# Kernel tuning notes

Hardware: AMD Instinct MI355X
Metric: run time of the kernel (lower is better)

Reference implementation:

```python
import jax, jax.numpy as jnp
import numpy as np

H, HKV, D, HID = 64, 8, 64, 2880
T = 2048
WINDOW = 128
THETA = 150000.0
FACTOR = 32.0
ORIG_MAX = 4096
BETA_FAST, BETA_SLOW = 32.0, 1.0
EPS = 1e-5
SCALE = D ** -0.5
MSCALE = float(0.1 * np.log(FACTOR) + 1.0)  # vLLM YaRN attention mscale


def _yarn_inv_freq():
    # vLLM YaRNScalingRotaryEmbedding inverse frequencies
    def corr_dim(n_rot):
        return D * np.log(ORIG_MAX / (n_rot * 2.0 * np.pi)) / (2.0 * np.log(THETA))
    low = max(int(np.floor(corr_dim(BETA_FAST))), 0)
    high = min(int(np.ceil(corr_dim(BETA_SLOW))), D - 1)
    pow_ = np.arange(0, D, 2, dtype=np.float32) / D
    extrap = 1.0 / (THETA ** pow_)                 # extrapolation inv_freq
    interp = extrap / FACTOR                        # interpolation inv_freq
    ramp = np.clip((np.arange(D // 2, dtype=np.float32) - low) / max(high - low, 1e-3), 0.0, 1.0)
    extrap_mask = 1.0 - ramp
    inv_freq = interp * (1.0 - extrap_mask) + extrap * extrap_mask
    return jnp.asarray(inv_freq, jnp.float32)

_INV_FREQ = _yarn_inv_freq()


def _rope(positions, x):
    # neox-style rotation; x: [T, heads, D]
    freqs = positions.astype(jnp.float32)[:, None] * _INV_FREQ[None, :]  # [T, D/2]
    cos = (jnp.cos(freqs) * MSCALE)[:, None, :]
    sin = (jnp.sin(freqs) * MSCALE)[:, None, :]
    x1, x2 = x[..., : D // 2], x[..., D // 2 :]
    return jnp.concatenate([x1 * cos - x2 * sin, x2 * cos + x1 * sin], axis=-1)


def _attn(q, k, v, sinks):
    # q: [T,H,D]; k,v: [T,HKV,D]; sinks: [H] extra softmax logit per head
    g = H // HKV
    k = jnp.repeat(k, g, axis=1)
    v = jnp.repeat(v, g, axis=1)
    scores = jnp.einsum('qhd,khd->hqk', q, k) * SCALE  # [H,T,T]
    i = jnp.arange(T)[:, None]
    j = jnp.arange(T)[None, :]
    mask = (j <= i) & (i - j < WINDOW)  # causal + sliding window (even layer)
    scores = jnp.where(mask[None], scores, -jnp.inf)
    s = sinks[:, None]                                    # [H,1]
    m = jnp.maximum(jnp.max(scores, axis=-1), s)          # [H,T]
    p = jnp.exp(scores - m[..., None])                    # [H,T,T]
    denom = jnp.sum(p, axis=-1) + jnp.exp(s - m)          # sink adds to denominator only
    out = jnp.einsum('hqk,khd->qhd', p, v) / denom.T[..., None]
    return out.reshape(T, H * D)


def setup_inputs() -> dict:
    key = jax.random.key(0)
    ks = jax.random.split(key, 8)
    return {
        'hidden_states': jax.random.normal(ks[0], (T, HID), jnp.float32),
        'positions': jnp.arange(T, dtype=jnp.int32),
        'norm_w': jnp.ones((HID,), jnp.float32),
        'w_qkv': jax.random.normal(ks[1], ((H + 2 * HKV) * D, HID), jnp.float32) * 0.02,
        'b_qkv': jax.random.normal(ks[2], ((H + 2 * HKV) * D,), jnp.float32) * 0.02,
        'w_o': jax.random.normal(ks[3], (HID, H * D), jnp.float32) * 0.02,
        'b_o': jax.random.normal(ks[4], (HID,), jnp.float32) * 0.02,
        'sinks': jax.random.normal(ks[5], (H,), jnp.float32),
    }


def reference(hidden_states, positions, norm_w, w_qkv, b_qkv, w_o, b_o, sinks):
    x = hidden_states
    t = x * jax.lax.rsqrt(jnp.mean(x * x, axis=-1, keepdims=True) + EPS) * norm_w  # RMSNorm
    qkv = t @ w_qkv.T + b_qkv
    q, k, v = jnp.split(qkv, [H * D, H * D + HKV * D], axis=-1)
    q = _rope(positions, q.reshape(T, H, D))
    k = _rope(positions, k.reshape(T, HKV, D))
    v = v.reshape(T, HKV, D)
    attn_out = _attn(q, k, v, sinks)
    out = attn_out @ w_o.T + b_o
    return out + x  # residual
```

## Files before the change

### kernel.cpp

```cpp
#include <hip/hip_runtime.h>
#include <hip/hip_bf16.h>
#include <stdint.h>

typedef __attribute__((ext_vector_type(8))) short bf16x8;
typedef __attribute__((ext_vector_type(8))) unsigned short u16x8;
typedef __attribute__((ext_vector_type(4))) float f32x4;
typedef __attribute__((ext_vector_type(4))) unsigned short u16x4;

#define T_SEQ 2048
#define HID_D 2880
#define KPAD 2944
#define NH 64
#define NKV 8
#define HD 64
#define QKV_N 5120
#define ATT_N 4096
#define NOPAD 3072
#define WIN 128
#define RSCALE 0.125f
#define MSCALE 1.3465735903f
#define ROPE_TOT (T_SEQ * (NH + NKV) * 32)

__device__ __forceinline__ unsigned short f2bf(float f) {
  union { float f; unsigned u; } v; v.f = f;
  unsigned r = v.u + 0x7fffu + ((v.u >> 16) & 1u);
  return (unsigned short)(r >> 16);
}
__device__ __forceinline__ float bf2f(unsigned short u) {
  union { unsigned u; float f; } v; v.u = ((unsigned)u) << 16;
  return v.f;
}

__device__ __forceinline__ void gload_lds16(const void* g, void* l) {
  __builtin_amdgcn_global_load_lds((const __attribute__((address_space(1))) char*)g,
                                   (__attribute__((address_space(3))) char*)l, 16, 0, 0);
}

#define GPH_MID()                                        \
  __builtin_amdgcn_s_barrier();                          \
  asm volatile("s_waitcnt lgkmcnt(0)" ::: "memory");     \
  __builtin_amdgcn_sched_barrier(0);                     \
  __builtin_amdgcn_s_setprio(1)
#define GPH_END()                                        \
  __builtin_amdgcn_s_setprio(0);                         \
  __builtin_amdgcn_s_barrier()

__global__ __launch_bounds__(256) void pre_kernel(const float* __restrict__ x,
                                                  const float* __restrict__ w,
                                                  unsigned short* __restrict__ t_bf,
                                                  const float* __restrict__ wq_src,
                                                  unsigned short* __restrict__ wq_dst) {
  __shared__ float red[256];
  if (blockIdx.x < 2048) {
    int row = blockIdx.x;
    const float4* xr4 = (const float4*)(x + (size_t)row * HID_D);
    const float4* w4 = (const float4*)w;
    float ss = 0.f;
    for (int i = threadIdx.x; i < 720; i += 256) {
      float4 v = xr4[i];
      ss += v.x * v.x + v.y * v.y + v.z * v.z + v.w * v.w;
    }
    red[threadIdx.x] = ss;
    __syncthreads();
    for (int s = 128; s > 0; s >>= 1) {
      if (threadIdx.x < s) red[threadIdx.x] += red[threadIdx.x + s];
      __syncthreads();
    }
    float rs = rsqrtf(red[0] / (float)HID_D + 1e-5f);
    u16x4* ob = (u16x4*)(t_bf + (size_t)row * KPAD);
    for (int i = threadIdx.x; i < 736; i += 256) {
      u16x4 o = {0, 0, 0, 0};
      if (i < 720) {
        float4 v = xr4[i];
        float4 g = w4[i];
        o = { f2bf(v.x * rs * g.x), f2bf(v.y * rs * g.y),
              f2bf(v.z * rs * g.z), f2bf(v.w * rs * g.w) };
      }
      ob[i] = o;
    }
  } else {
    const int total = QKV_N * 736;
    for (int i = (blockIdx.x - 2048) * 256 + threadIdx.x; i < total; i += 1024 * 256) {
      int c4 = i % 736, row = i / 736;
      u16x4 o = {0, 0, 0, 0};
      if (c4 < 720) {
        float4 v = ((const float4*)wq_src)[(size_t)row * 720 + c4];
        o = { f2bf(v.x), f2bf(v.y), f2bf(v.z), f2bf(v.w) };
      }
      ((u16x4*)wq_dst)[i] = o;
    }
  }
}

__global__ __launch_bounds__(512, 2) void qkv320_kernel(const unsigned short* __restrict__ A,
                                                        const unsigned short* __restrict__ B,
                                                        unsigned short* __restrict__ C,
                                                        const float* __restrict__ bias) {
  __shared__ unsigned short sA[2 * 128 * 64];
  __shared__ unsigned short sB[3 * 320 * 64];

  const int tid = threadIdx.x;
  const int lane = tid & 63, wid = tid >> 6;
  const int wr = wid >> 2, wc = wid & 3;
  const int lq = lane & 15, ro = lane >> 4;

  const int c = blockIdx.x & 7, q = blockIdx.x >> 3;
  const int by = (c & 1) * 8 + (q & 7);
  const int bx = (c >> 1) * 4 + (q >> 3);
  const int m0 = by * 128, n0 = bx * 320;

  const int R0 = tid >> 3;
  const int g0 = (((tid & 7) ^ (R0 & 7)) << 3);
  const size_t aOff = (size_t)(m0 + R0) * KPAD + g0;
  size_t bOff[5];
#pragma unroll
  for (int r = 0; r < 5; ++r)
    bOff[r] = (size_t)(n0 + r * 64 + R0) * KPAD + g0;

  const int ck0 = ((ro ^ (lq & 7)) << 3);
  const int ck1 = (((4 + ro) ^ (lq & 7)) << 3);

#define QSTG_A(BUF, KT)                                                         \
  { unsigned short* _d = sA + (BUF) * 8192 + wid * 512;                         \
    const unsigned short* _s = A + aOff + (size_t)(KT) * 64;                    \
    gload_lds16(_s, _d); gload_lds16(_s + (size_t)64 * KPAD, _d + 4096); }
#define QSTG_B(BUF, KT)                                                         \
  { unsigned short* _d = sB + (BUF) * 20480 + wid * 512;                        \
    gload_lds16(B + bOff[0] + (KT) * 64, _d);                                   \
    gload_lds16(B + bOff[1] + (KT) * 64, _d + 4096);                            \
    gload_lds16(B + bOff[2] + (KT) * 64, _d + 8192);                            \
    gload_lds16(B + bOff[3] + (KT) * 64, _d + 12288);                           \
    gload_lds16(B + bOff[4] + (KT) * 64, _d + 16384); }

  bf16x8 aR[8];
  bf16x8 b00, b01, b10, b11, b20, b21, b30, b31, b40, b41;
  f32x4 acc[4][5] = {};

#define QLDA(BUF)                                                                          \
  { _Pragma("unroll") for (int ii = 0; ii < 4; ++ii) {                                     \
      const int _r = (BUF) * 8192 + (wr * 64 + ii * 16 + lq) * 64;                         \
      aR[ii * 2 + 0] = *(const bf16x8*)&sA[_r + ck0];                                      \
      aR[ii * 2 + 1] = *(const bf16x8*)&sA[_r + ck1]; } }
#define QLDB(BUF, J, D0, D1)                                                               \
  { const int _r = (BUF) * 20480 + (wc * 80 + (J) * 16 + lq) * 64;                         \
    D0 = *(const bf16x8*)&sB[_r + ck0];                                                    \
    D1 = *(const bf16x8*)&sB[_r + ck1]; }
#define QMM(J, B0, B1)                                                                     \
  { _Pragma("unroll") for (int ii = 0; ii < 4; ++ii) {                                     \
      acc[ii][J] = __builtin_amdgcn_mfma_f32_16x16x32_bf16(aR[ii * 2 + 0], B0, acc[ii][J], 0, 0, 0); \
      acc[ii][J] = __builtin_amdgcn_mfma_f32_16x16x32_bf16(aR[ii * 2 + 1], B1, acc[ii][J], 0, 0, 0); } }

  QSTG_B(0, 0); QSTG_A(0, 0);
  QSTG_B(1, 1); QSTG_A(1, 1);
  asm volatile("s_waitcnt vmcnt(7)" ::: "memory");
  __builtin_amdgcn_s_barrier();

  const int nt = 46;
  for (int T = 0; T < nt; ++T) {
    const bool more = (T + 2 < nt);
    const int bb = T % 3, bA = T & 1;
    QLDA(bA);
    QLDB(bb, 0, b00, b01);
    QLDB(bb, 1, b10, b11);
    if (more) QSTG_B((T + 2) % 3, T + 2);
    GPH_MID();
    QMM(0, b00, b01);
    QMM(1, b10, b11);
    GPH_END();
    QLDB(bb, 2, b20, b21);
    QLDB(bb, 3, b30, b31);
    QLDB(bb, 4, b40, b41);
    if (more) QSTG_A((T + 2) & 1, T + 2);
    GPH_MID();
    QMM(2, b20, b21);
    QMM(3, b30, b31);
    QMM(4, b40, b41);
    __builtin_amdgcn_s_setprio(0);
    if (more) asm volatile("s_waitcnt vmcnt(7)" ::: "memory");
    else      asm volatile("s_waitcnt vmcnt(0)" ::: "memory");
    __builtin_amdgcn_s_barrier();
  }
#undef QSTG_A
#undef QSTG_B
#undef QLDA
#undef QLDB
#undef QMM

#pragma unroll
  for (int ii = 0; ii < 4; ++ii) {
    const int gr = m0 + wr * 64 + ii * 16 + ro * 4;
#pragma unroll
    for (int j = 0; j < 5; ++j) {
      const int gc = n0 + wc * 80 + j * 16 + lq;
      const float bv = bias[gc];
#pragma unroll
      for (int r = 0; r < 4; ++r)
        C[(size_t)(gr + r) * QKV_N + gc] = f2bf(acc[ii][j][r] + bv);
    }
  }
}

__global__ __launch_bounds__(512, 2) void outproj192_kernel(const unsigned short* __restrict__ att,
                                                            const unsigned short* __restrict__ wo,
                                                            float* __restrict__ out,
                                                            const float* __restrict__ b_o,
                                                            const float* __restrict__ x) {
  __shared__ unsigned short sA[3 * 128 * 64];
  __shared__ unsigned short sB[3 * 192 * 64];

  const int tid = threadIdx.x;
  const int lane = tid & 63, wid = tid >> 6;
  const int wr = wid >> 2, wc = wid & 3;
  const int lq = lane & 15, ro = lane >> 4;

  const int c = blockIdx.x & 7, q = blockIdx.x >> 3;
  const int by = c * 2 + (q >= 15 ? 1 : 0);
  const int bx = (q >= 15) ? q - 15 : q;
  const int m0 = by * 128, n0 = bx * 192;

  const int R0 = tid >> 3;
  const int g0 = (((tid & 7) ^ (R0 & 7)) << 3);
  const size_t aOff = (size_t)(m0 + R0) * ATT_N + g0;
  size_t bOff[3];
#pragma unroll
  for (int r = 0; r < 3; ++r)
    bOff[r] = (size_t)(n0 + r * 64 + R0) * ATT_N + g0;

  const int ck0 = ((ro ^ (lq & 7)) << 3);
  const int ck1 = (((4 + ro) ^ (lq & 7)) << 3);

#define PSTG_A(BUF, KT)                                                         \
  { unsigned short* _d = sA + (BUF) * 8192 + wid * 512;                         \
    const unsigned short* _s = att + aOff + (size_t)(KT) * 64;                  \
    gload_lds16(_s, _d); gload_lds16(_s + (size_t)64 * ATT_N, _d + 4096); }
#define PSTG_B(BUF, KT)                                                         \
  { unsigned short* _d = sB + (BUF) * 12288 + wid * 512;                        \
    gload_lds16(wo + bOff[0] + (KT) * 64, _d);                                  \
    gload_lds16(wo + bOff[1] + (KT) * 64, _d + 4096);                           \
    gload_lds16(wo + bOff[2] + (KT) * 64, _d + 8192); }

  bf16x8 aR[8];
  bf16x8 b00, b01, b10, b11, b20, b21;
  f32x4 acc[4][3] = {};

#define PLDA(BUF)                                                                          \
  { _Pragma("unroll") for (int ii = 0; ii < 4; ++ii) {                                     \
      const int _r = (BUF) * 8192 + (wr * 64 + ii * 16 + lq) * 64;                         \
      aR[ii * 2 + 0] = *(const bf16x8*)&sA[_r + ck0];                                      \
      aR[ii * 2 + 1] = *(const bf16x8*)&sA[_r + ck1]; } }
#define PLDB(BUF, J, D0, D1)                                                               \
  { const int _r = (BUF) * 12288 + (wc * 48 + (J) * 16 + lq) * 64;                         \
    D0 = *(const bf16x8*)&sB[_r + ck0];                                                    \
    D1 = *(const bf16x8*)&sB[_r + ck1]; }

  PSTG_B(0, 0); PSTG_A(0, 0);
  PSTG_B(1, 1); PSTG_A(1, 1);
  asm volatile("s_waitcnt vmcnt(5)" ::: "memory");
  __builtin_amdgcn_s_barrier();

  const int nt = 64;
  for (int T = 0; T < nt; ++T) {
    const bool more = (T + 2 < nt);
    const int bb = T % 3;
    PLDA(bb);
    PLDB(bb, 0, b00, b01);
    PLDB(bb, 1, b10, b11);
    PLDB(bb, 2, b20, b21);
    if (more) { PSTG_B((T + 2) % 3, T + 2); PSTG_A((T + 2) % 3, T + 2); }
    GPH_MID();
#pragma unroll
    for (int ii = 0; ii < 4; ++ii) {
      acc[ii][0] = __builtin_amdgcn_mfma_f32_16x16x32_bf16(aR[ii * 2 + 0], b00, acc[ii][0], 0, 0, 0);
      acc[ii][0] = __builtin_amdgcn_mfma_f32_16x16x32_bf16(aR[ii * 2 + 1], b01, acc[ii][0], 0, 0, 0);
      acc[ii][1] = __builtin_amdgcn_mfma_f32_16x16x32_bf16(aR[ii * 2 + 0], b10, acc[ii][1], 0, 0, 0);
      acc[ii][1] = __builtin_amdgcn_mfma_f32_16x16x32_bf16(aR[ii * 2 + 1], b11, acc[ii][1], 0, 0, 0);
      acc[ii][2] = __builtin_amdgcn_mfma_f32_16x16x32_bf16(aR[ii * 2 + 0], b20, acc[ii][2], 0, 0, 0);
      acc[ii][2] = __builtin_amdgcn_mfma_f32_16x16x32_bf16(aR[ii * 2 + 1], b21, acc[ii][2], 0, 0, 0);
    }
    __builtin_amdgcn_s_setprio(0);
    if (more) asm volatile("s_waitcnt vmcnt(5)" ::: "memory");
    else      asm volatile("s_waitcnt vmcnt(0)" ::: "memory");
    __builtin_amdgcn_s_barrier();
  }
#undef PSTG_A
#undef PSTG_B
#undef PLDA
#undef PLDB

#pragma unroll
  for (int ii = 0; ii < 4; ++ii) {
    const int gr = m0 + wr * 64 + ii * 16 + ro * 4;
#pragma unroll
    for (int j = 0; j < 3; ++j) {
      const int gc = n0 + wc * 48 + j * 16 + lq;
      const float bv = b_o[gc];
#pragma unroll
      for (int r = 0; r < 4; ++r) {
        size_t off = (size_t)(gr + r) * HID_D + gc;
        out[off] = acc[ii][j][r] + bv + x[off];
      }
    }
  }
}

__global__ __launch_bounds__(256) void ropev_kernel(const unsigned short* __restrict__ qkvb,
                                                    const int* __restrict__ positions,
                                                    unsigned short* __restrict__ qb,
                                                    unsigned short* __restrict__ kb) {
  int idx = blockIdx.x * 256 + threadIdx.x;
  int d = idx & 31;
  int head = (idx >> 5) % (NH + NKV);
  int t = idx / ((NH + NKV) * 32);
  float pw = (float)d * (1.0f / 32.0f);
  float extrap = expf(-pw * 11.9183905733f);
  float interp = extrap * (1.0f / 32.0f);
  float ramp = fminf(fmaxf(((float)d - 8.0f) * 0.1f, 0.0f), 1.0f);
  float invf = interp * ramp + extrap * (1.0f - ramp);
  float fr = (float)positions[t] * invf;
  float s, c;
  sincosf(fr, &s, &c);
  c *= MSCALE;
  s *= MSCALE;
  if (head < NH) {
    const unsigned short* b = qkvb + (size_t)t * QKV_N + head * HD + d;
    float x1 = bf2f(b[0]), x2 = bf2f(b[32]);
    unsigned short* ob = qb + (size_t)t * ATT_N + head * HD + d;
    ob[0] = f2bf(x1 * c - x2 * s);
    ob[32] = f2bf(x2 * c + x1 * s);
  } else {
    int gk = head - NH;
    const unsigned short* b = qkvb + (size_t)t * QKV_N + NH * HD + gk * HD + d;
    float x1 = bf2f(b[0]), x2 = bf2f(b[32]);
    unsigned short* ob = kb + (size_t)t * (NKV * HD) + gk * HD + d;
    ob[0] = f2bf(x1 * c - x2 * s);
    ob[32] = f2bf(x2 * c + x1 * s);
  }
}

__global__ __launch_bounds__(256) void vtrans_kernel(const unsigned short* __restrict__ qkvb,
                                                     unsigned short* __restrict__ vt) {
  __shared__ unsigned short tile[64][72];
  const int g = blockIdx.x >> 5;
  const int t0 = (blockIdx.x & 31) << 6;
  const int r = threadIdx.x >> 3;
  const int c8 = (threadIdx.x & 7) << 3;
  const size_t vbase = (size_t)(NH + NKV) * HD + (size_t)g * HD;
#pragma unroll
  for (int hh = 0; hh < 2; ++hh) {
    int row = r + hh * 32;
    *(u16x8*)&tile[row][c8] =
        *(const u16x8*)(qkvb + (size_t)(t0 + row) * QKV_N + vbase + c8);
  }
  __syncthreads();
  const int d = threadIdx.x >> 2;
  const int ts = (threadIdx.x & 3) << 4;
  u16x8 v0, v1;
#pragma unroll
  for (int i = 0; i < 8; ++i) { v0[i] = tile[ts + i][d]; v1[i] = tile[ts + 8 + i][d]; }
  unsigned short* dst = vt + (size_t)(g * HD + d) * T_SEQ + t0 + ts;
  *(u16x8*)dst = v0;
  *(u16x8*)(dst + 8) = v1;
}

__global__ __launch_bounds__(256) void attn_kernel(const unsigned short* __restrict__ qb,
                                                   const unsigned short* __restrict__ kb,
                                                   const unsigned short* __restrict__ vt,
                                                   const float* __restrict__ sinks,
                                                   unsigned short* __restrict__ att,
                                                   const float* __restrict__ wo_src,
                                                   unsigned short* __restrict__ wo_dst) {
  __shared__ unsigned short orep[4][16][72];
  {
    const int bid = blockIdx.y * gridDim.x + blockIdx.x;
    const int total = HID_D * 1024;
    for (int i = bid * 256 + threadIdx.x; i < total; i += 2048 * 256) {
      float4 v = ((const float4*)wo_src)[i];
      u16x4 o = { f2bf(v.x), f2bf(v.y), f2bf(v.z), f2bf(v.w) };
      ((u16x4*)wo_dst)[i] = o;
    }
  }
  const int lane = threadIdx.x & 63;
  const int wid = threadIdx.x >> 6;
  const int q0 = blockIdx.x * 16;
  const int h = blockIdx.y * 4 + wid;
  const int g = h >> 3;
  const int lq = lane & 15;
  const int ro = lane >> 4;

  bf16x8 bq0, bq1;
  {
    const unsigned short* qp = qb + (size_t)(q0 + lq) * ATT_N + h * HD + ro * 8;
    bq0 = *(const bf16x8*)qp;
    bq1 = *(const bf16x8*)(qp + 32);
  }
  float m_run = sinks[h];
  float l_run = 1.0f;
  f32x4 o0 = {0.f, 0.f, 0.f, 0.f}, o1 = o0, o2 = o0, o3 = o0;
  const int qg = q0 + lq;
  const int jstart = (q0 >= WIN) ? q0 - WIN : 0;

  for (int jt = jstart; jt <= q0; jt += 32) {
    f32x4 st0 = {0.f, 0.f, 0.f, 0.f}, st1 = st0;
    {
      int kr = jt + ((lq >> 2) << 3) + (lq & 3);
      int kr0 = min(kr, T_SEQ - 1);
      int kr1 = min(kr + 4, T_SEQ - 1);
      const unsigned short* kp0 = kb + (size_t)kr0 * (NKV * HD) + g * HD + ro * 8;
      const unsigned short* kp1 = kb + (size_t)kr1 * (NKV * HD) + g * HD + ro * 8;
      bf16x8 ka0a = *(const bf16x8*)kp0;
      bf16x8 ka0b = *(const bf16x8*)(kp0 + 32);
      bf16x8 ka1a = *(const bf16x8*)kp1;
      bf16x8 ka1b = *(const bf16x8*)(kp1 + 32);
      st0 = __builtin_amdgcn_mfma_f32_16x16x32_bf16(ka0a, bq0, st0, 0, 0, 0);
      st0 = __builtin_amdgcn_mfma_f32_16x16x32_bf16(ka0b, bq1, st0, 0, 0, 0);
      st1 = __builtin_amdgcn_mfma_f32_16x16x32_bf16(ka1a, bq0, st1, 0, 0, 0);
      st1 = __builtin_amdgcn_mfma_f32_16x16x32_bf16(ka1b, bq1, st1, 0, 0, 0);
    }
    float p[8];
    float tmax = -3.0e30f;
#pragma unroll
    for (int r = 0; r < 4; ++r) {
      int jg0 = jt + ro * 8 + r;
      int jg1 = jg0 + 4;
      float s0 = (jg0 <= qg && (qg - jg0) < WIN) ? st0[r] * RSCALE : -3.0e30f;
      float s1 = (jg1 <= qg && (qg - jg1) < WIN) ? st1[r] * RSCALE : -3.0e30f;
      p[r] = s0;
      p[r + 4] = s1;
      tmax = fmaxf(tmax, fmaxf(s0, s1));
    }
    tmax = fmaxf(tmax, __shfl_xor(tmax, 16));
    tmax = fmaxf(tmax, __shfl_xor(tmax, 32));
    float m_new = fmaxf(m_run, tmax);
    float rescale = expf(m_run - m_new);
    float psum = 0.f;
    bf16x8 pa;
#pragma unroll
    for (int jj = 0; jj < 8; ++jj) {
      float pe = expf(p[jj] - m_new);
      psum += pe;
      pa[jj] = (short)f2bf(pe);
    }
    psum += __shfl_xor(psum, 16);
    psum += __shfl_xor(psum, 32);
    l_run = l_run * rescale + psum;
    m_run = m_new;
    f32x4 rs4;
#pragma unroll
    for (int r = 0; r < 4; ++r) rs4[r] = __shfl(rescale, ro * 4 + r);
    o0 *= rs4; o1 *= rs4; o2 *= rs4; o3 *= rs4;
    int tb = jt + ro * 8;
    if (tb > T_SEQ - 8) tb = T_SEQ - 8;
    const unsigned short* vp = vt + (size_t)(g * HD + lq) * T_SEQ + tb;
    bf16x8 v0 = *(const bf16x8*)vp;
    bf16x8 v1 = *(const bf16x8*)(vp + 16 * T_SEQ);
    bf16x8 v2 = *(const bf16x8*)(vp + 32 * T_SEQ);
    bf16x8 v3 = *(const bf16x8*)(vp + 48 * T_SEQ);
    o0 = __builtin_amdgcn_mfma_f32_16x16x32_bf16(pa, v0, o0, 0, 0, 0);
    o1 = __builtin_amdgcn_mfma_f32_16x16x32_bf16(pa, v1, o1, 0, 0, 0);
    o2 = __builtin_amdgcn_mfma_f32_16x16x32_bf16(pa, v2, o2, 0, 0, 0);
    o3 = __builtin_amdgcn_mfma_f32_16x16x32_bf16(pa, v3, o3, 0, 0, 0);
  }

#pragma unroll
  for (int r = 0; r < 4; ++r) {
    float lr = __shfl(l_run, ro * 4 + r);
    float inv = 1.0f / lr;
    int row = ro * 4 + r;
    orep[wid][row][lq]      = f2bf(o0[r] * inv);
    orep[wid][row][lq + 16] = f2bf(o1[r] * inv);
    orep[wid][row][lq + 32] = f2bf(o2[r] * inv);
    orep[wid][row][lq + 48] = f2bf(o3[r] * inv);
  }
  {
    const int row = lane >> 2;
    const int seg = (lane & 3) << 4;
    u16x8 w0 = *(const u16x8*)&orep[wid][row][seg];
    u16x8 w1 = *(const u16x8*)&orep[wid][row][seg + 8];
    unsigned short* op = att + (size_t)(q0 + row) * ATT_N + h * HD + seg;
    *(u16x8*)op = w0;
    *(u16x8*)(op + 8) = w1;
  }
}

extern "C" void kernel_launch(void* const* d_in, const int* in_sizes, int n_in,
                              void* d_out, int out_size, void* d_ws, size_t ws_size,
                              hipStream_t stream) {
  const float* x = (const float*)d_in[0];
  const int* pos = (const int*)d_in[1];
  const float* norm_w = (const float*)d_in[2];
  const float* w_qkv = (const float*)d_in[3];
  const float* b_qkv = (const float*)d_in[4];
  const float* w_o = (const float*)d_in[5];
  const float* b_o = (const float*)d_in[6];
  const float* sinks = (const float*)d_in[7];
  float* out = (float*)d_out;

  unsigned short* t_bf = (unsigned short*)d_ws;
  unsigned short* wq_bf = t_bf + (size_t)T_SEQ * KPAD;
  unsigned short* wo_bf = wq_bf + (size_t)QKV_N * KPAD;
  unsigned short* qkv_bf = wo_bf + (size_t)NOPAD * ATT_N;
  unsigned short* qb = qkv_bf + (size_t)T_SEQ * QKV_N;
  unsigned short* kb = qb + (size_t)T_SEQ * ATT_N;
  unsigned short* vt = kb + (size_t)T_SEQ * NKV * HD;
  unsigned short* att = vt + (size_t)NKV * HD * T_SEQ;

  pre_kernel<<<3072, 256, 0, stream>>>(x, norm_w, t_bf, w_qkv, wq_bf);
  qkv320_kernel<<<256, 512, 0, stream>>>(t_bf, wq_bf, qkv_bf, b_qkv);
  ropev_kernel<<<ROPE_TOT / 256, 256, 0, stream>>>(qkv_bf, pos, qb, kb);
  vtrans_kernel<<<256, 256, 0, stream>>>(qkv_bf, vt);
  attn_kernel<<<dim3(T_SEQ / 16, NH / 4), 256, 0, stream>>>(qb, kb, vt, sinks, att, w_o, wo_bf);
  outproj192_kernel<<<240, 512, 0, stream>>>(att, wo_bf, out, b_o, x);
}
```

Measured before the change: 221.4 us.

## Rework out-projection GEMM to double-buffered K=128 tiles and fuse V transpose into RoPE

The output projection GEMM moves from a triple-buffered pipeline with K=64 tiles to a double-buffered one with K=128 tiles. That halves the number of loop iterations and barriers, and each iteration runs two MFMA phases with explicit lgkmcnt waits and raised wave priority. It also waits vmcnt(0) every iteration instead of keeping two stages in flight. Separately, the V-transpose kernel is merged into the RoPE kernel as extra blocks, removing one launch. Shared memory use in the GEMM rises (2x128x128 + 2x192x128 bf16, 160 KB), which may limit occupancy to one block per CU.

```diff
diff --git a/kernel.cpp b/kernel.cpp
--- a/kernel.cpp
+++ b/kernel.cpp
@@ -20,6 +20,7 @@
 #define RSCALE 0.125f
 #define MSCALE 1.3465735903f
 #define ROPE_TOT (T_SEQ * (NH + NKV) * 32)
+#define ROPE_BLKS (ROPE_TOT / 256)
 
 __device__ __forceinline__ unsigned short f2bf(float f) {
   union { float f; unsigned u; } v; v.f = f;
@@ -205,8 +206,8 @@
                                                             float* __restrict__ out,
                                                             const float* __restrict__ b_o,
                                                             const float* __restrict__ x) {
-  __shared__ unsigned short sA[3 * 128 * 64];
-  __shared__ unsigned short sB[3 * 192 * 64];
+  __shared__ unsigned short sA[2 * 128 * 128];
+  __shared__ unsigned short sB[2 * 192 * 128];
 
   const int tid = threadIdx.x;
   const int lane = tid & 63, wid = tid >> 6;
@@ -218,74 +219,79 @@
   const int bx = (q >= 15) ? q - 15 : q;
   const int m0 = by * 128, n0 = bx * 192;
 
-  const int R0 = tid >> 3;
-  const int g0 = (((tid & 7) ^ (R0 & 7)) << 3);
-  const size_t aOff = (size_t)(m0 + R0) * ATT_N + g0;
-  size_t bOff[3];
-#pragma unroll
-  for (int r = 0; r < 3; ++r)
-    bOff[r] = (size_t)(n0 + r * 64 + R0) * ATT_N + g0;
-
-  const int ck0 = ((ro ^ (lq & 7)) << 3);
-  const int ck1 = (((4 + ro) ^ (lq & 7)) << 3);
-
-#define PSTG_A(BUF, KT)                                                         \
-  { unsigned short* _d = sA + (BUF) * 8192 + wid * 512;                         \
-    const unsigned short* _s = att + aOff + (size_t)(KT) * 64;                  \
-    gload_lds16(_s, _d); gload_lds16(_s + (size_t)64 * ATT_N, _d + 4096); }
-#define PSTG_B(BUF, KT)                                                         \
-  { unsigned short* _d = sB + (BUF) * 12288 + wid * 512;                        \
-    gload_lds16(wo + bOff[0] + (KT) * 64, _d);                                  \
-    gload_lds16(wo + bOff[1] + (KT) * 64, _d + 4096);                           \
-    gload_lds16(wo + bOff[2] + (KT) * 64, _d + 8192); }
+  const int SR = tid >> 4;
+  const int g0 = (((tid & 15) ^ (SR & 7)) << 3);
+  const size_t aOff = (size_t)(m0 + SR) * ATT_N + g0;
+  const size_t bOffBase = (size_t)(n0 + SR) * ATT_N + g0;
+
+  const int ck00 = (((0 + ro) ^ (lq & 7)) << 3);
+  const int ck01 = (((4 + ro) ^ (lq & 7)) << 3);
+  const int ck10 = (((8 + ro) ^ (lq & 7)) << 3);
+  const int ck11 = (((12 + ro) ^ (lq & 7)) << 3);
+
+#define OSTG(BUF, KT)                                                             \
+  { _Pragma("unroll") for (int ci = 0; ci < 4; ++ci)                              \
+      gload_lds16(att + aOff + (size_t)(ci * 32) * ATT_N + (KT) * 128,            \
+                  sA + (BUF) * 16384 + ci * 4096 + tid * 8);                      \
+    _Pragma("unroll") for (int ci = 0; ci < 6; ++ci)                              \
+      gload_lds16(wo + bOffBase + (size_t)(ci * 32) * ATT_N + (KT) * 128,         \
+                  sB + (BUF) * 24576 + ci * 4096 + tid * 8); }
 
   bf16x8 aR[8];
   bf16x8 b00, b01, b10, b11, b20, b21;
   f32x4 acc[4][3] = {};
 
-#define PLDA(BUF)                                                                          \
+#define OLDA(BUF, C0, C1)                                                                  \
   { _Pragma("unroll") for (int ii = 0; ii < 4; ++ii) {                                     \
-      const int _r = (BUF) * 8192 + (wr * 64 + ii * 16 + lq) * 64;                         \
-      aR[ii * 2 + 0] = *(const bf16x8*)&sA[_r + ck0];                                      \
-      aR[ii * 2 + 1] = *(const bf16x8*)&sA[_r + ck1]; } }
-#define PLDB(BUF, J, D0, D1)                                                               \
-  { const int _r = (BUF) * 12288 + (wc * 48 + (J) * 16 + lq) * 64;                         \
-    D0 = *(const bf16x8*)&sB[_r + ck0];                                                    \
-    D1 = *(const bf16x8*)&sB[_r + ck1]; }
-
-  PSTG_B(0, 0); PSTG_A(0, 0);
-  PSTG_B(1, 1); PSTG_A(1, 1);
-  asm volatile("s_waitcnt vmcnt(5)" ::: "memory");
+      const int _r = (BUF) * 16384 + (wr * 64 + ii * 16 + lq) * 128;                       \
+      aR[ii * 2 + 0] = *(const bf16x8*)&sA[_r + C0];                                       \
+      aR[ii * 2 + 1] = *(const bf16x8*)&sA[_r + C1]; } }
+#define OLDB(BUF, J, C0, C1, D0, D1)                                                       \
+  { const int _r = (BUF) * 24576 + (wc * 48 + (J) * 16 + lq) * 128;                        \
+    D0 = *(const bf16x8*)&sB[_r + C0];                                                     \
+    D1 = *(const bf16x8*)&sB[_r + C1]; }
+#define OMM()                                                                              \
+  { _Pragma("unroll") for (int ii = 0; ii < 4; ++ii) {                                     \
+      acc[ii][0] = __builtin_amdgcn_mfma_f32_16x16x32_bf16(aR[ii * 2 + 0], b00, acc[ii][0], 0, 0, 0); \
+      acc[ii][0] = __builtin_amdgcn_mfma_f32_16x16x32_bf16(aR[ii * 2 + 1], b01, acc[ii][0], 0, 0, 0); \
+      acc[ii][1] = __builtin_amdgcn_mfma_f32_16x16x32_bf16(aR[ii * 2 + 0], b10, acc[ii][1], 0, 0, 0); \
+      acc[ii][1] = __builtin_amdgcn_mfma_f32_16x16x32_bf16(aR[ii * 2 + 1], b11, acc[ii][1], 0, 0, 0); \
+      acc[ii][2] = __builtin_amdgcn_mfma_f32_16x16x32_bf16(aR[ii * 2 + 0], b20, acc[ii][2], 0, 0, 0); \
+      acc[ii][2] = __builtin_amdgcn_mfma_f32_16x16x32_bf16(aR[ii * 2 + 1], b21, acc[ii][2], 0, 0, 0); } }
+
+  OSTG(0, 0);
+  asm volatile("s_waitcnt vmcnt(0)" ::: "memory");
   __builtin_amdgcn_s_barrier();
 
-  const int nt = 64;
+  const int nt = 32;
   for (int T = 0; T < nt; ++T) {
-    const bool more = (T + 2 < nt);
-    const int bb = T % 3;
-    PLDA(bb);
-    PLDB(bb, 0, b00, b01);
-    PLDB(bb, 1, b10, b11);
-    PLDB(bb, 2, b20, b21);
-    if (more) { PSTG_B((T + 2) % 3, T + 2); PSTG_A((T + 2) % 3, T + 2); }
-    GPH_MID();
-#pragma unroll
-    for (int ii = 0; ii < 4; ++ii) {
-      acc[ii][0] = __builtin_amdgcn_mfma_f32_16x16x32_bf16(aR[ii * 2 + 0], b00, acc[ii][0], 0, 0, 0);
-      acc[ii][0] = __builtin_amdgcn_mfma_f32_16x16x32_bf16(aR[ii * 2 + 1], b01, acc[ii][0], 0, 0, 0);
-      acc[ii][1] = __builtin_amdgcn_mfma_f32_16x16x32_bf16(aR[ii * 2 + 0], b10, acc[ii][1], 0, 0, 0);
-      acc[ii][1] = __builtin_amdgcn_mfma_f32_16x16x32_bf16(aR[ii * 2 + 1], b11, acc[ii][1], 0, 0, 0);
-      acc[ii][2] = __builtin_amdgcn_mfma_f32_16x16x32_bf16(aR[ii * 2 + 0], b20, acc[ii][2], 0, 0, 0);
-      acc[ii][2] = __builtin_amdgcn_mfma_f32_16x16x32_bf16(aR[ii * 2 + 1], b21, acc[ii][2], 0, 0, 0);
-    }
+    const int bb = T & 1;
+    if (T + 1 < nt) OSTG(bb ^ 1, T + 1);
+    OLDA(bb, ck00, ck01);
+    OLDB(bb, 0, ck00, ck01, b00, b01);
+    OLDB(bb, 1, ck00, ck01, b10, b11);
+    OLDB(bb, 2, ck00, ck01, b20, b21);
+    asm volatile("s_waitcnt lgkmcnt(0)" ::: "memory");
+    __builtin_amdgcn_sched_barrier(0);
+    __builtin_amdgcn_s_setprio(1);
+    OMM();
     __builtin_amdgcn_s_setprio(0);
-    if (more) asm volatile("s_waitcnt vmcnt(5)" ::: "memory");
-    else      asm volatile("s_waitcnt vmcnt(0)" ::: "memory");
+    OLDA(bb, ck10, ck11);
+    OLDB(bb, 0, ck10, ck11, b00, b01);
+    OLDB(bb, 1, ck10, ck11, b10, b11);
+    OLDB(bb, 2, ck10, ck11, b20, b21);
+    asm volatile("s_waitcnt lgkmcnt(0)" ::: "memory");
+    __builtin_amdgcn_sched_barrier(0);
+    __builtin_amdgcn_s_setprio(1);
+    OMM();
+    __builtin_amdgcn_s_setprio(0);
+    asm volatile("s_waitcnt vmcnt(0)" ::: "memory");
     __builtin_amdgcn_s_barrier();
   }
-#undef PSTG_A
-#undef PSTG_B
-#undef PLDA
-#undef PLDB
+#undef OSTG
+#undef OLDA
+#undef OLDB
+#undef OMM
 
 #pragma unroll
   for (int ii = 0; ii < 4; ++ii) {
@@ -303,10 +309,36 @@
   }
 }
 
-__global__ __launch_bounds__(256) void ropev_kernel(const unsigned short* __restrict__ qkvb,
-                                                    const int* __restrict__ positions,
-                                                    unsigned short* __restrict__ qb,
-                                                    unsigned short* __restrict__ kb) {
+__global__ __launch_bounds__(256) void ropevt_kernel(const unsigned short* __restrict__ qkvb,
+                                                     const int* __restrict__ positions,
+                                                     unsigned short* __restrict__ qb,
+                                                     unsigned short* __restrict__ kb,
+                                                     unsigned short* __restrict__ vt) {
+  __shared__ unsigned short tile[64][72];
+  if (blockIdx.x >= ROPE_BLKS) {
+    const int vb = blockIdx.x - ROPE_BLKS;
+    const int g = vb >> 5;
+    const int t0 = (vb & 31) << 6;
+    const int r = threadIdx.x >> 3;
+    const int c8 = (threadIdx.x & 7) << 3;
+    const size_t vbase = (size_t)(NH + NKV) * HD + (size_t)g * HD;
+#pragma unroll
+    for (int hh = 0; hh < 2; ++hh) {
+      int row = r + hh * 32;
+      *(u16x8*)&tile[row][c8] =
+          *(const u16x8*)(qkvb + (size_t)(t0 + row) * QKV_N + vbase + c8);
+    }
+    __syncthreads();
+    const int d = threadIdx.x >> 2;
+    const int ts = (threadIdx.x & 3) << 4;
+    u16x8 v0, v1;
+#pragma unroll
+    for (int i = 0; i < 8; ++i) { v0[i] = tile[ts + i][d]; v1[i] = tile[ts + 8 + i][d]; }
+    unsigned short* dst = vt + (size_t)(g * HD + d) * T_SEQ + t0 + ts;
+    *(u16x8*)dst = v0;
+    *(u16x8*)(dst + 8) = v1;
+    return;
+  }
   int idx = blockIdx.x * 256 + threadIdx.x;
   int d = idx & 31;
   int head = (idx >> 5) % (NH + NKV);
@@ -337,31 +369,6 @@
   }
 }
 
-__global__ __launch_bounds__(256) void vtrans_kernel(const unsigned short* __restrict__ qkvb,
-                                                     unsigned short* __restrict__ vt) {
-  __shared__ unsigned short tile[64][72];
-  const int g = blockIdx.x >> 5;
-  const int t0 = (blockIdx.x & 31) << 6;
-  const int r = threadIdx.x >> 3;
-  const int c8 = (threadIdx.x & 7) << 3;
-  const size_t vbase = (size_t)(NH + NKV) * HD + (size_t)g * HD;
-#pragma unroll
-  for (int hh = 0; hh < 2; ++hh) {
-    int row = r + hh * 32;
-    *(u16x8*)&tile[row][c8] =
-        *(const u16x8*)(qkvb + (size_t)(t0 + row) * QKV_N + vbase + c8);
-  }
-  __syncthreads();
-  const int d = threadIdx.x >> 2;
-  const int ts = (threadIdx.x & 3) << 4;
-  u16x8 v0, v1;
-#pragma unroll
-  for (int i = 0; i < 8; ++i) { v0[i] = tile[ts + i][d]; v1[i] = tile[ts + 8 + i][d]; }
-  unsigned short* dst = vt + (size_t)(g * HD + d) * T_SEQ + t0 + ts;
-  *(u16x8*)dst = v0;
-  *(u16x8*)(dst + 8) = v1;
-}
-
 __global__ __launch_bounds__(256) void attn_kernel(const unsigned short* __restrict__ qb,
                                                    const unsigned short* __restrict__ kb,
                                                    const unsigned short* __restrict__ vt,
@@ -506,8 +513,7 @@
 
   pre_kernel<<<3072, 256, 0, stream>>>(x, norm_w, t_bf, w_qkv, wq_bf);
   qkv320_kernel<<<256, 512, 0, stream>>>(t_bf, wq_bf, qkv_bf, b_qkv);
-  ropev_kernel<<<ROPE_TOT / 256, 256, 0, stream>>>(qkv_bf, pos, qb, kb);
-  vtrans_kernel<<<256, 256, 0, stream>>>(qkv_bf, vt);
+  ropevt_kernel<<<ROPE_BLKS + 256, 256, 0, stream>>>(qkv_bf, pos, qb, kb, vt);
   attn_kernel<<<dim3(T_SEQ / 16, NH / 4), 256, 0, stream>>>(qb, kb, vt, sinks, att, w_o, wo_bf);
   outproj192_kernel<<<240, 512, 0, stream>>>(att, wo_bf, out, b_o, x);
 }
```

New measurement: 230.0 us. 1.04x slower.
